# Performance work log

Hardware: AMD Instinct MI355X
Metric: run time of the kernel (lower is better)

The kernel has to match this reference:

```python
import jax, jax.numpy as jnp
import numpy as np

MARGIN = 0.5  # init kwarg 'margin'
TWO_N, D = 8192, 256


def setup_inputs() -> dict:
    key = jax.random.key(0)
    k1, k2 = jax.random.split(key)
    embeddings = jax.random.normal(k1, (TWO_N, D), dtype=jnp.float32)
    neg_mask = jax.random.bernoulli(k2, 0.5, (TWO_N, TWO_N))  # bool [2N, 2N]
    return {"embeddings": embeddings, "neg_mask": neg_mask}


def _cdist(x, y):
    # Euclidean pairwise distances via the Gram trick (matches torch.cdist p=2)
    x2 = jnp.sum(x * x, axis=-1)[:, None]
    y2 = jnp.sum(y * y, axis=-1)[None, :]
    sq = jnp.maximum(x2 + y2 - 2.0 * (x @ y.T), 0.0)
    return jnp.sqrt(sq + 1e-12)


def reference(embeddings, neg_mask):
    two_n = embeddings.shape[0]
    n = two_n // 2
    d = _cdist(embeddings, embeddings)  # [2N, 2N]
    # masked sum of exp(margin - d) per anchor row (vectorizes the python loop)
    exp_neg = jnp.where(neg_mask, jnp.exp(MARGIN - d), 0.0)
    row_sums = exp_neg.sum(axis=1)  # [2N]
    idx = jnp.arange(n)
    ap = d[idx, idx + n]  # anchor-positive distances [N]
    j = jnp.log(row_sums[:n] + row_sums[n:]) + ap  # [N]
    # original skips NaN entries before the mean
    valid = ~jnp.isnan(j)
    r2 = jnp.where(valid, jnp.square(jnp.maximum(j, 0.0)), 0.0)
    cnt = jnp.maximum(valid.sum(), 1).astype(r2.dtype)
    loss = r2.sum() / cnt / 2.0
    return loss
```

## Files before the change

### kernel.cpp

```cpp
#include <hip/hip_runtime.h>
#include <hip/hip_bf16.h>
#include <stdint.h>

#define TWO_N  8192
#define NHALF  4096
#define DDIM   256
#define MARGIN 0.5f
#define NTRI   2080

static const size_t OFF_EMB  = 0;
static const size_t OFF_X2   = 4u * 1024 * 1024;
static const size_t OFF_AP   = OFF_X2 + (size_t)TWO_N * 4;
static const size_t OFF_FLAG = OFF_AP + (size_t)NHALF * 4;
static const size_t OFF_BITM = 5u * 1024 * 1024;
static const size_t OFF_RS   = 13u * 1024 * 1024;

typedef __attribute__((ext_vector_type(8))) short bf16x8;
typedef __attribute__((ext_vector_type(4))) float f32x4;

__device__ inline ushort f2bf(float f) {
  uint32_t u = __float_as_uint(f);
  uint32_t r = (u + 0x7FFFu + ((u >> 16) & 1u)) >> 16;
  return (ushort)r;
}
__device__ inline float bf2f(ushort h) { return __uint_as_float((uint32_t)h << 16); }

__device__ inline void gload_lds16(const void* g, void* l) {
  __builtin_amdgcn_global_load_lds(
      (const __attribute__((address_space(1))) uint32_t*)(uintptr_t)g,
      (__attribute__((address_space(3))) uint32_t*)(uint32_t)(uintptr_t)l,
      16, 0, 0);
}
__device__ inline void gload_lds4(const void* g, void* l) {
  __builtin_amdgcn_global_load_lds(
      (const __attribute__((address_space(1))) uint32_t*)(uintptr_t)g,
      (__attribute__((address_space(3))) uint32_t*)(uint32_t)(uintptr_t)l,
      4, 0, 0);
}

__global__ __launch_bounds__(256) void smv2_prep(
    const float* __restrict__ emb,
    const uint32_t* __restrict__ maskw,
    ushort* __restrict__ emb_bf,
    float* __restrict__ x2,
    int* __restrict__ flag)
{
  const int t = threadIdx.x;
  if (blockIdx.x == 0) {
    __shared__ int sflag;
    if (t == 0) sflag = 0;
    __syncthreads();
    int found = 0;
    #pragma unroll
    for (int k = 0; k < 8; ++k) {
      uint32_t w = maskw[t * 8 + k];
      if (w > 1u && (w & 0xFEFEFEFEu) == 0u) found = 1;
    }
    if (found) atomicOr(&sflag, 1);
    __syncthreads();
    if (t == 0) *flag = sflag;
  }
  const int row  = blockIdx.x * 8 + (t >> 5);
  const int lane = t & 31;
  const float* rp = emb + (size_t)row * DDIM + lane * 8;
  float4 v0 = *(const float4*)(rp);
  float4 v1 = *(const float4*)(rp + 4);
  float vals[8] = {v0.x, v0.y, v0.z, v0.w, v1.x, v1.y, v1.z, v1.w};
  uint32_t packed[4];
  float ss = 0.f;
  #pragma unroll
  for (int k = 0; k < 4; ++k) {
    ushort h0 = f2bf(vals[2 * k]);
    ushort h1 = f2bf(vals[2 * k + 1]);
    packed[k] = (uint32_t)h0 | ((uint32_t)h1 << 16);
    float f0 = bf2f(h0), f1 = bf2f(h1);
    ss += f0 * f0 + f1 * f1;
  }
  *(uint4*)(emb_bf + (size_t)row * DDIM + lane * 8) =
      make_uint4(packed[0], packed[1], packed[2], packed[3]);
  #pragma unroll
  for (int m = 1; m < 32; m <<= 1) ss += __shfl_xor(ss, m);
  if (lane == 0) x2[row] = ss;
}

__global__ __launch_bounds__(256) void smv2_pack(
    const uint8_t* __restrict__ mask8,
    const int* __restrict__ flagp,
    uint32_t* __restrict__ bitM,
    float* __restrict__ rs)
{
  const int t = threadIdx.x;
  if (blockIdx.x == 0) {
    float4 z = {0.f, 0.f, 0.f, 0.f};
    #pragma unroll
    for (int i = 0; i < 8; ++i) ((float4*)rs)[t * 8 + i] = z;
  }
  const int tid = blockIdx.x * 256 + t;
  const int isByte = *flagp;
  if (isByte) {
    #pragma unroll
    for (int it = 0; it < 4; ++it) {
      const int idx = it * (2048 * 256) + tid;
      const uint4 a = ((const uint4*)mask8)[(size_t)idx * 2];
      const uint4 b = ((const uint4*)mask8)[(size_t)idx * 2 + 1];
      const uint32_t wsv[8] = {a.x, a.y, a.z, a.w, b.x, b.y, b.z, b.w};
      uint32_t out = 0;
      #pragma unroll
      for (int j = 0; j < 8; ++j)
        out |= ((((wsv[j] & 0x01010101u) * 0x01020408u) >> 24) & 0xFu) << (4 * j);
      bitM[idx] = out;
    }
  } else {
    const uint32_t* maskw = (const uint32_t*)mask8;
    #pragma unroll
    for (int it = 0; it < 4; ++it) {
      const int idx = it * (2048 * 256) + tid;
      uint32_t out = 0;
      #pragma unroll
      for (int j = 0; j < 8; ++j) {
        const uint4 wv = ((const uint4*)maskw)[(size_t)idx * 8 + j];
        out |= (wv.x != 0u ? 1u : 0u) << (4 * j);
        out |= (wv.y != 0u ? 1u : 0u) << (4 * j + 1);
        out |= (wv.z != 0u ? 1u : 0u) << (4 * j + 2);
        out |= (wv.w != 0u ? 1u : 0u) << (4 * j + 3);
      }
      bitM[idx] = out;
    }
  }
}

__global__ __launch_bounds__(512, 8) void smv2_main(
    const ushort* __restrict__ emb_bf,
    const float* __restrict__ x2,
    const uint8_t* __restrict__ bitM,
    float* __restrict__ ap,
    float* __restrict__ rs)
{
  __shared__ char bufA[2 * 8192];
  __shared__ char bufB[2 * 8192];
  __shared__ uint32_t ldsM[512];
  __shared__ float ldsX[256];

  const int t = threadIdx.x;

  const int bid = blockIdx.x;
  const int idx = (bid & 7) * (NTRI / 8) + (bid >> 3);
  float rf = sqrtf(8.f * (float)idx + 1.f);
  int bx = (int)((rf - 1.f) * 0.5f);
  while ((bx + 1) * (bx + 2) / 2 <= idx) ++bx;
  while (bx * (bx + 1) / 2 > idx) --bx;
  const int by = idx - bx * (bx + 1) / 2;
  const int brow = by * 128;
  const int bcol = bx * 128;
  const bool diag = (bx == by);

  const char* gA = (const char*)(emb_bf + (size_t)brow * DDIM);
  const char* gB = (const char*)(emb_bf + (size_t)bcol * DDIM);

  const int srow = t >> 2;
  const int scb  = ((t & 3) * 16) ^ (((srow >> 1) & 3) << 4);
  const size_t gOff = (size_t)srow * 512 + scb;
  const int ldst = t * 16;

  const int w  = t >> 6;
  const int l  = t & 63;
  const int wr = w >> 2;
  const int wc = w & 3;
  const int cl = l & 15;
  const int kh = l >> 4;

  int aoff[4], boff[2];
  #pragma unroll
  for (int m = 0; m < 4; ++m) {
    const int row = wr * 64 + m * 16 + cl;
    aoff[m] = row * 64 + ((kh * 16) ^ (((row >> 1) & 3) << 4));
  }
  #pragma unroll
  for (int n = 0; n < 2; ++n) {
    const int row = wc * 32 + n * 16 + cl;
    boff[n] = row * 64 + ((kh * 16) ^ (((row >> 1) & 3) << 4));
  }

  f32x4 acc[4][2];
  #pragma unroll
  for (int m = 0; m < 4; ++m)
    #pragma unroll
    for (int n = 0; n < 2; ++n) {
      f32x4 z = {0.f, 0.f, 0.f, 0.f};
      acc[m][n] = z;
    }

  uint2 m2[2];
  #pragma unroll
  for (int n = 0; n < 2; ++n) {
    const int gj = bcol + wc * 32 + n * 16 + cl;
    m2[n] = *(const uint2*)(bitM + (size_t)gj * 1024 + (brow >> 3) + wr * 8);
  }
  __builtin_amdgcn_sched_barrier(0);

  gload_lds4(bitM + (size_t)(brow + srow) * 1024 + (bcol >> 3) + (t & 3) * 4,
             (char*)ldsM + t * 4);
  {
    const int xi = t & 255;
    const float* src = (xi < 128) ? (x2 + brow + xi) : (x2 + bcol + (xi - 128));
    gload_lds4(src, (char*)ldsX + xi * 4);
  }
  gload_lds16(gA + gOff, bufA + ldst);
  gload_lds16(gB + gOff, bufB + ldst);
  __syncthreads();

#define STAGE(Q)                                                            \
  {                                                                         \
    gload_lds16(gA + gOff + (Q) * 64, bufA + ((Q) & 1) * 8192 + ldst);      \
    gload_lds16(gB + gOff + (Q) * 64, bufB + ((Q) & 1) * 8192 + ldst);      \
  }

#define COMPUTE(P)                                                          \
  {                                                                         \
    const char* ba = bufA + ((P) & 1) * 8192;                               \
    const char* bb = bufB + ((P) & 1) * 8192;                               \
    bf16x8 a0 = *(const bf16x8*)(ba + aoff[0]);                             \
    bf16x8 a1 = *(const bf16x8*)(ba + aoff[1]);                             \
    bf16x8 a2 = *(const bf16x8*)(ba + aoff[2]);                             \
    bf16x8 a3 = *(const bf16x8*)(ba + aoff[3]);                             \
    bf16x8 b0 = *(const bf16x8*)(bb + boff[0]);                             \
    bf16x8 b1 = *(const bf16x8*)(bb + boff[1]);                             \
    acc[0][0] = __builtin_amdgcn_mfma_f32_16x16x32_bf16(a0, b0, acc[0][0], 0, 0, 0); \
    acc[0][1] = __builtin_amdgcn_mfma_f32_16x16x32_bf16(a0, b1, acc[0][1], 0, 0, 0); \
    acc[1][0] = __builtin_amdgcn_mfma_f32_16x16x32_bf16(a1, b0, acc[1][0], 0, 0, 0); \
    acc[1][1] = __builtin_amdgcn_mfma_f32_16x16x32_bf16(a1, b1, acc[1][1], 0, 0, 0); \
    acc[2][0] = __builtin_amdgcn_mfma_f32_16x16x32_bf16(a2, b0, acc[2][0], 0, 0, 0); \
    acc[2][1] = __builtin_amdgcn_mfma_f32_16x16x32_bf16(a2, b1, acc[2][1], 0, 0, 0); \
    acc[3][0] = __builtin_amdgcn_mfma_f32_16x16x32_bf16(a3, b0, acc[3][0], 0, 0, 0); \
    acc[3][1] = __builtin_amdgcn_mfma_f32_16x16x32_bf16(a3, b1, acc[3][1], 0, 0, 0); \
  }

#define PHASE(P)                                                            \
  {                                                                         \
    if ((P) < 7) STAGE((P) + 1);                                            \
    __builtin_amdgcn_sched_barrier(0);                                      \
    COMPUTE(P);                                                             \
    __syncthreads();                                                        \
  }

  PHASE(0) PHASE(1) PHASE(2) PHASE(3) PHASE(4) PHASE(5) PHASE(6) PHASE(7)

  float* part  = (float*)bufA;
  float* part2 = (float*)bufB;
  float cs[2] = {0.f, 0.f};

  #pragma unroll
  for (int m = 0; m < 4; ++m) {
    #pragma unroll
    for (int q = 0; q < 4; ++q) {
      const int lrow = wr * 64 + m * 16 + kh * 4 + q;
      const int gi = brow + lrow;
      const float xi = ldsX[lrow];
      const uint32_t m1w = ldsM[lrow * 4 + wc];
      float rp = 0.f;
      #pragma unroll
      for (int n = 0; n < 2; ++n) {
        const int jc = wc * 32 + n * 16 + cl;
        const int gj = bcol + jc;
        const float g = acc[m][n][q];
        float sq = (gi == gj) ? 0.f : (xi + ldsX[128 + jc] - 2.f * g);
        sq = fmaxf(sq, 0.f) + 1e-12f;
        const float dd = __builtin_amdgcn_sqrtf(sq);
        if (gj == gi + NHALF && gi < NHALF) ap[gi] = dd;
        const float e = __expf(MARGIN - dd);
        const uint32_t mk1 = (m1w >> (n * 16 + cl)) & 1u;
        rp += mk1 ? e : 0.f;
        const uint32_t m2bits = (m < 2) ? m2[n].x : m2[n].y;
        const uint32_t mk2 = (m2bits >> ((m & 1) * 16 + kh * 4 + q)) & 1u;
        cs[n] += mk2 ? e : 0.f;
      }
      #pragma unroll
      for (int s = 1; s < 16; s <<= 1) rp += __shfl_xor(rp, s);
      if (cl == 0) part[wc * 128 + lrow] = rp;
    }
  }

  #pragma unroll
  for (int n = 0; n < 2; ++n) {
    cs[n] += __shfl_xor(cs[n], 16);
    cs[n] += __shfl_xor(cs[n], 32);
    if (l < 16) part2[wr * 128 + wc * 32 + n * 16 + l] = cs[n];
  }
  __syncthreads();

  if (t < 128) {
    atomicAdd(&rs[brow + t],
              (part[t] + part[128 + t]) + (part[256 + t] + part[384 + t]));
    if (!diag)
      atomicAdd(&rs[bcol + t], part2[t] + part2[128 + t]);
  }
#undef PHASE
#undef COMPUTE
#undef STAGE
}

__global__ __launch_bounds__(1024) void smv2_finalize(
    const float* __restrict__ rs, const float* __restrict__ ap,
    float* __restrict__ out)
{
  const int t = threadIdx.x;
  float sum = 0.f, cnt = 0.f;
  for (int i = t; i < NHALF; i += 1024) {
    float rsum = rs[i] + rs[i + NHALF];
    float jv = logf(rsum) + ap[i];
    if (!isnan(jv)) {
      cnt += 1.f;
      float mj = fmaxf(jv, 0.f);
      sum += mj * mj;
    }
  }
  __shared__ float ssum[16], scnt[16];
  #pragma unroll
  for (int s = 32; s >= 1; s >>= 1) {
    sum += __shfl_down(sum, s);
    cnt += __shfl_down(cnt, s);
  }
  const int wid = t >> 6, lid = t & 63;
  if (lid == 0) { ssum[wid] = sum; scnt[wid] = cnt; }
  __syncthreads();
  if (t == 0) {
    float S = 0.f, C = 0.f;
    #pragma unroll
    for (int i = 0; i < 16; ++i) { S += ssum[i]; C += scnt[i]; }
    if (C < 1.f) C = 1.f;
    out[0] = S / C * 0.5f;
  }
}

extern "C" void kernel_launch(void* const* d_in, const int* in_sizes, int n_in,
                              void* d_out, int out_size, void* d_ws, size_t ws_size,
                              hipStream_t stream) {
  const float* emb = (const float*)d_in[0];
  const void* mask = d_in[1];
  char* ws = (char*)d_ws;

  ushort*   emb_bf = (ushort*)(ws + OFF_EMB);
  float*    x2     = (float*)(ws + OFF_X2);
  float*    ap     = (float*)(ws + OFF_AP);
  int*      flag   = (int*)(ws + OFF_FLAG);
  uint32_t* bitM   = (uint32_t*)(ws + OFF_BITM);
  float*    rs     = (float*)(ws + OFF_RS);

  smv2_prep<<<1024, 256, 0, stream>>>(emb, (const uint32_t*)mask, emb_bf, x2, flag);
  smv2_pack<<<2048, 256, 0, stream>>>((const uint8_t*)mask, flag, bitM, rs);
  smv2_main<<<NTRI, 512, 0, stream>>>(emb_bf, x2, (const uint8_t*)bitM, ap, rs);
  smv2_finalize<<<1, 1024, 0, stream>>>(rs, ap, (float*)d_out);
}
```

Before: 441.9 us.

## Load GEMM operands directly from global into registers, dropping LDS staging

Replaces the double-buffered global-to-LDS staging of embedding tiles with direct per-lane global loads of bf16x8 fragments feeding the MFMAs. This removes eight barriers per tile and most of the LDS footprint, relying on L1/L2 caching for the reuse across waves. The occupancy hint in launch bounds is lowered from 8 to 6. The trade-off is redundant global/L2 traffic, since each wave now fetches A and B fragments independently, and the loads are no longer overlapped with compute by explicit double buffering.

```diff
diff --git a/kernel.cpp b/kernel.cpp
--- a/kernel.cpp
+++ b/kernel.cpp
@@ -25,12 +25,6 @@
 }
 __device__ inline float bf2f(ushort h) { return __uint_as_float((uint32_t)h << 16); }
 
-__device__ inline void gload_lds16(const void* g, void* l) {
-  __builtin_amdgcn_global_load_lds(
-      (const __attribute__((address_space(1))) uint32_t*)(uintptr_t)g,
-      (__attribute__((address_space(3))) uint32_t*)(uint32_t)(uintptr_t)l,
-      16, 0, 0);
-}
 __device__ inline void gload_lds4(const void* g, void* l) {
   __builtin_amdgcn_global_load_lds(
       (const __attribute__((address_space(1))) uint32_t*)(uintptr_t)g,
@@ -129,17 +123,17 @@
   }
 }
 
-__global__ __launch_bounds__(512, 8) void smv2_main(
+__global__ __launch_bounds__(512, 6) void smv2_main(
     const ushort* __restrict__ emb_bf,
     const float* __restrict__ x2,
     const uint8_t* __restrict__ bitM,
     float* __restrict__ ap,
     float* __restrict__ rs)
 {
-  __shared__ char bufA[2 * 8192];
-  __shared__ char bufB[2 * 8192];
   __shared__ uint32_t ldsM[512];
   __shared__ float ldsX[256];
+  __shared__ float part[512];
+  __shared__ float part2[256];
 
   const int t = threadIdx.x;
 
@@ -154,49 +148,13 @@
   const int bcol = bx * 128;
   const bool diag = (bx == by);
 
-  const char* gA = (const char*)(emb_bf + (size_t)brow * DDIM);
-  const char* gB = (const char*)(emb_bf + (size_t)bcol * DDIM);
-
-  const int srow = t >> 2;
-  const int scb  = ((t & 3) * 16) ^ (((srow >> 1) & 3) << 4);
-  const size_t gOff = (size_t)srow * 512 + scb;
-  const int ldst = t * 16;
-
   const int w  = t >> 6;
   const int l  = t & 63;
   const int wr = w >> 2;
   const int wc = w & 3;
   const int cl = l & 15;
   const int kh = l >> 4;
-
-  int aoff[4], boff[2];
-  #pragma unroll
-  for (int m = 0; m < 4; ++m) {
-    const int row = wr * 64 + m * 16 + cl;
-    aoff[m] = row * 64 + ((kh * 16) ^ (((row >> 1) & 3) << 4));
-  }
-  #pragma unroll
-  for (int n = 0; n < 2; ++n) {
-    const int row = wc * 32 + n * 16 + cl;
-    boff[n] = row * 64 + ((kh * 16) ^ (((row >> 1) & 3) << 4));
-  }
-
-  f32x4 acc[4][2];
-  #pragma unroll
-  for (int m = 0; m < 4; ++m)
-    #pragma unroll
-    for (int n = 0; n < 2; ++n) {
-      f32x4 z = {0.f, 0.f, 0.f, 0.f};
-      acc[m][n] = z;
-    }
-
-  uint2 m2[2];
-  #pragma unroll
-  for (int n = 0; n < 2; ++n) {
-    const int gj = bcol + wc * 32 + n * 16 + cl;
-    m2[n] = *(const uint2*)(bitM + (size_t)gj * 1024 + (brow >> 3) + wr * 8);
-  }
-  __builtin_amdgcn_sched_barrier(0);
+  const int srow = t >> 2;
 
   gload_lds4(bitM + (size_t)(brow + srow) * 1024 + (bcol >> 3) + (t & 3) * 4,
              (char*)ldsM + t * 4);
@@ -205,48 +163,45 @@
     const float* src = (xi < 128) ? (x2 + brow + xi) : (x2 + bcol + (xi - 128));
     gload_lds4(src, (char*)ldsX + xi * 4);
   }
-  gload_lds16(gA + gOff, bufA + ldst);
-  gload_lds16(gB + gOff, bufB + ldst);
+  uint2 m2[2];
+  #pragma unroll
+  for (int n = 0; n < 2; ++n) {
+    const int gj = bcol + wc * 32 + n * 16 + cl;
+    m2[n] = *(const uint2*)(bitM + (size_t)gj * 1024 + (brow >> 3) + wr * 8);
+  }
+
+  const char* pA = (const char*)emb_bf + (size_t)(brow + wr * 64 + cl) * 512 + kh * 16;
+  const char* pB = (const char*)emb_bf + (size_t)(bcol + wc * 32 + cl) * 512 + kh * 16;
+
+  f32x4 acc[4][2];
+  #pragma unroll
+  for (int m = 0; m < 4; ++m)
+    #pragma unroll
+    for (int n = 0; n < 2; ++n) {
+      f32x4 z = {0.f, 0.f, 0.f, 0.f};
+      acc[m][n] = z;
+    }
+
+  #pragma unroll
+  for (int p = 0; p < 8; ++p) {
+    bf16x8 a0 = *(const bf16x8*)(pA + 0 * 8192 + p * 64);
+    bf16x8 a1 = *(const bf16x8*)(pA + 1 * 8192 + p * 64);
+    bf16x8 a2 = *(const bf16x8*)(pA + 2 * 8192 + p * 64);
+    bf16x8 a3 = *(const bf16x8*)(pA + 3 * 8192 + p * 64);
+    bf16x8 b0 = *(const bf16x8*)(pB + 0 * 8192 + p * 64);
+    bf16x8 b1 = *(const bf16x8*)(pB + 1 * 8192 + p * 64);
+    acc[0][0] = __builtin_amdgcn_mfma_f32_16x16x32_bf16(a0, b0, acc[0][0], 0, 0, 0);
+    acc[0][1] = __builtin_amdgcn_mfma_f32_16x16x32_bf16(a0, b1, acc[0][1], 0, 0, 0);
+    acc[1][0] = __builtin_amdgcn_mfma_f32_16x16x32_bf16(a1, b0, acc[1][0], 0, 0, 0);
+    acc[1][1] = __builtin_amdgcn_mfma_f32_16x16x32_bf16(a1, b1, acc[1][1], 0, 0, 0);
+    acc[2][0] = __builtin_amdgcn_mfma_f32_16x16x32_bf16(a2, b0, acc[2][0], 0, 0, 0);
+    acc[2][1] = __builtin_amdgcn_mfma_f32_16x16x32_bf16(a2, b1, acc[2][1], 0, 0, 0);
+    acc[3][0] = __builtin_amdgcn_mfma_f32_16x16x32_bf16(a3, b0, acc[3][0], 0, 0, 0);
+    acc[3][1] = __builtin_amdgcn_mfma_f32_16x16x32_bf16(a3, b1, acc[3][1], 0, 0, 0);
+  }
+
   __syncthreads();
 
-#define STAGE(Q)                                                            \
-  {                                                                         \
-    gload_lds16(gA + gOff + (Q) * 64, bufA + ((Q) & 1) * 8192 + ldst);      \
-    gload_lds16(gB + gOff + (Q) * 64, bufB + ((Q) & 1) * 8192 + ldst);      \
-  }
-
-#define COMPUTE(P)                                                          \
-  {                                                                         \
-    const char* ba = bufA + ((P) & 1) * 8192;                               \
-    const char* bb = bufB + ((P) & 1) * 8192;                               \
-    bf16x8 a0 = *(const bf16x8*)(ba + aoff[0]);                             \
-    bf16x8 a1 = *(const bf16x8*)(ba + aoff[1]);                             \
-    bf16x8 a2 = *(const bf16x8*)(ba + aoff[2]);                             \
-    bf16x8 a3 = *(const bf16x8*)(ba + aoff[3]);                             \
-    bf16x8 b0 = *(const bf16x8*)(bb + boff[0]);                             \
-    bf16x8 b1 = *(const bf16x8*)(bb + boff[1]);                             \
-    acc[0][0] = __builtin_amdgcn_mfma_f32_16x16x32_bf16(a0, b0, acc[0][0], 0, 0, 0); \
-    acc[0][1] = __builtin_amdgcn_mfma_f32_16x16x32_bf16(a0, b1, acc[0][1], 0, 0, 0); \
-    acc[1][0] = __builtin_amdgcn_mfma_f32_16x16x32_bf16(a1, b0, acc[1][0], 0, 0, 0); \
-    acc[1][1] = __builtin_amdgcn_mfma_f32_16x16x32_bf16(a1, b1, acc[1][1], 0, 0, 0); \
-    acc[2][0] = __builtin_amdgcn_mfma_f32_16x16x32_bf16(a2, b0, acc[2][0], 0, 0, 0); \
-    acc[2][1] = __builtin_amdgcn_mfma_f32_16x16x32_bf16(a2, b1, acc[2][1], 0, 0, 0); \
-    acc[3][0] = __builtin_amdgcn_mfma_f32_16x16x32_bf16(a3, b0, acc[3][0], 0, 0, 0); \
-    acc[3][1] = __builtin_amdgcn_mfma_f32_16x16x32_bf16(a3, b1, acc[3][1], 0, 0, 0); \
-  }
-
-#define PHASE(P)                                                            \
-  {                                                                         \
-    if ((P) < 7) STAGE((P) + 1);                                            \
-    __builtin_amdgcn_sched_barrier(0);                                      \
-    COMPUTE(P);                                                             \
-    __syncthreads();                                                        \
-  }
-
-  PHASE(0) PHASE(1) PHASE(2) PHASE(3) PHASE(4) PHASE(5) PHASE(6) PHASE(7)
-
-  float* part  = (float*)bufA;
-  float* part2 = (float*)bufB;
   float cs[2] = {0.f, 0.f};
 
   #pragma unroll
@@ -294,9 +249,6 @@
     if (!diag)
       atomicAdd(&rs[bcol + t], part2[t] + part2[128 + t]);
   }
-#undef PHASE
-#undef COMPUTE
-#undef STAGE
 }
 
 __global__ __launch_bounds__(1024) void smv2_finalize(
```

After: 490.3 us. 10.9% more time.
